# Kernel tuning notes

Hardware: AMD Instinct MI355X
Metric: run time of the kernel (lower is better)

## Reference

```python
import jax, jax.numpy as jnp
import numpy as np

IN_CH = 4096
OUT_CH = 4096
DENSITY = 0.1
BATCH = 8192


def setup_inputs() -> dict:
    key = jax.random.key(0)
    k_mask, k_w, k_b, k_x = jax.random.split(key, 4)
    # Fixed sparsity pattern, as in the torch module's sparse_mask.nonzero()
    mask = jax.random.bernoulli(k_mask, DENSITY, (OUT_CH, IN_CH))
    rows, cols = jnp.nonzero(mask)  # unique (row, col) pairs
    rows = rows.astype(jnp.int32)
    cols = cols.astype(jnp.int32)
    nnz = rows.shape[0]
    # Kaiming-style init per output row (approximate: uniform bound from mean fan-in)
    fan_in = jnp.maximum(jnp.sum(mask, axis=1).astype(jnp.float32), 1.0)  # [OUT_CH]
    gain = np.sqrt(2.0 / (1.0 + 5.0))  # leaky_relu gain with a=sqrt(5)
    std = gain / jnp.sqrt(fan_in)
    w_bound = np.sqrt(3.0) * std  # per-row bound
    u = jax.random.uniform(k_w, (nnz,), minval=-1.0, maxval=1.0)
    sparse_weight = u * w_bound[rows]
    b_bound = 1.0 / jnp.sqrt(fan_in)
    bias = jax.random.uniform(k_b, (OUT_CH,), minval=-1.0, maxval=1.0) * b_bound
    x = jax.random.normal(k_x, (BATCH, IN_CH), dtype=jnp.float32)
    return {
        "x": x,
        "sparse_weight": sparse_weight.astype(jnp.float32),
        "rows": rows,
        "cols": cols,
        "bias": bias.astype(jnp.float32),
    }


def reference(x, sparse_weight, rows, cols, bias):
    # Rebuild the (fixed-pattern) sparse weight as a dense [OUT_CH, IN_CH] matrix
    # (indices are unique, so .set matches the COO semantics), then y = x @ W^T + b.
    W = jnp.zeros((OUT_CH, IN_CH), dtype=sparse_weight.dtype).at[rows, cols].set(sparse_weight)
    return x @ W.T + bias  # [BATCH, OUT_CH]
```

## Files before the change

kernel.cpp:

```cpp
#include <hip/hip_runtime.h>
#include <hip/hip_bf16.h>

#define M_DIM 8192
#define N_DIM 4096
#define K_DIM 4096
#define BM 256
#define BN 128
#define BK 64
#define A_ELEMS (BM * BK)
#define B_ELEMS (BN * BK)
#define LDS_BYTES ((3 * (A_ELEMS + B_ELEMS)) * 2)
#define NT_TILES (K_DIM / BK)

typedef __bf16 bf16x8 __attribute__((ext_vector_type(8)));
typedef float  f32x4  __attribute__((ext_vector_type(4)));
typedef unsigned short u16x8 __attribute__((ext_vector_type(8)));

#define ASYNC16(g, l)                                                          \
  __builtin_amdgcn_global_load_lds(                                            \
      (__attribute__((address_space(1))) void*)(g),                            \
      (__attribute__((address_space(3))) void*)(l), 16, 0, 0)

static __device__ __forceinline__ unsigned short f2bf(float f) {
  unsigned int u = __float_as_uint(f);
  u += 0x7fffu + ((u >> 16) & 1u);
  return (unsigned short)(u >> 16);
}

__global__ __launch_bounds__(256) void sl_prep_bs(
    const float4* __restrict__ x4, u16x8* __restrict__ xb,
    const float* __restrict__ vals, const int* __restrict__ rows,
    const int* __restrict__ cols, unsigned short* __restrict__ W, int nnz) {
  const int b = blockIdx.x;
  if (b < N_DIM) {
    __shared__ __align__(16) unsigned short rowbuf[K_DIM];
    u16x8* rb8 = (u16x8*)rowbuf;
    u16x8 z = {};
    rb8[threadIdx.x] = z;
    rb8[256 + threadIdx.x] = z;
    __syncthreads();
    int l = 0, h = nnz;
    while (l < h) { int m = (l + h) >> 1; if (rows[m] < b) l = m + 1; else h = m; }
    const int s = l;
    h = nnz;
    while (l < h) { int m = (l + h) >> 1; if (rows[m] <= b) l = m + 1; else h = m; }
    const int e = l;
    for (int k = s + threadIdx.x; k < e; k += 256)
      rowbuf[cols[k]] = f2bf(vals[k]);
    __syncthreads();
    u16x8* dst = (u16x8*)(W + (size_t)b * K_DIM);
    dst[threadIdx.x] = rb8[threadIdx.x];
    dst[256 + threadIdx.x] = rb8[256 + threadIdx.x];
  } else {
    const int i = (b - N_DIM) * 256 + threadIdx.x;
    float4 a = x4[2 * i];
    float4 c = x4[2 * i + 1];
    u16x8 o;
    o[0] = f2bf(a.x); o[1] = f2bf(a.y); o[2] = f2bf(a.z); o[3] = f2bf(a.w);
    o[4] = f2bf(c.x); o[5] = f2bf(c.y); o[6] = f2bf(c.z); o[7] = f2bf(c.w);
    xb[i] = o;
  }
}

__global__ __launch_bounds__(512, 2) void sl_gemm_bias(
    const unsigned short* __restrict__ A,
    const unsigned short* __restrict__ B,
    const float* __restrict__ bias,
    float* __restrict__ C) {
  extern __shared__ __align__(16) unsigned short lds[];
  unsigned short* As = lds;
  unsigned short* Bs = lds + 3 * A_ELEMS;

  const int tid  = threadIdx.x;
  const int wave = tid >> 6;
  const int lane = tid & 63;

  const int orig = blockIdx.y * (M_DIM / BM) + blockIdx.x;
  const int swz  = (orig & 7) * 128 + (orig >> 3);
  const int mt   = swz >> 5;
  const int nt   = swz & 31;
  const int m0 = mt * BM;
  const int n0 = nt * BN;

  const int srow = tid >> 3;
  const int scol = ((tid & 7) ^ (srow & 7)) * 8;
  const unsigned short* gA = A + (size_t)(m0 + srow) * K_DIM + scol;
  const unsigned short* gB = B + (size_t)(n0 + srow) * K_DIM + scol;
  const size_t GROW = (size_t)64 * K_DIM;
  const int ldsw = wave * 64 * 8;

  const int wm   = (wave >> 2) * 128;
  const int wn   = (wave & 3) * 32;
  const int fm   = lane & 15;
  const int quad = lane >> 4;
  int offA[8], offB[2], pk[2];
#pragma unroll
  for (int i = 0; i < 8; ++i) offA[i] = (wm + i * 16 + fm) * BK;
#pragma unroll
  for (int i = 0; i < 2; ++i) offB[i] = (wn + i * 16 + fm) * BK;
#pragma unroll
  for (int i = 0; i < 2; ++i) pk[i] = ((i * 4 + quad) ^ (fm & 7)) * 8;

  f32x4 acc[8][2] = {};

#pragma unroll
  for (int tt = 0; tt < 2; ++tt) {
#pragma unroll
    for (int r = 0; r < 4; ++r)
      ASYNC16(gA + tt * BK + r * GROW, As + tt * A_ELEMS + ldsw + r * 4096);
#pragma unroll
    for (int r = 0; r < 2; ++r)
      ASYNC16(gB + tt * BK + r * GROW, Bs + tt * B_ELEMS + ldsw + r * 4096);
  }
  gA += 2 * BK;
  gB += 2 * BK;
  asm volatile("s_waitcnt vmcnt(6)" ::: "memory");
  __builtin_amdgcn_sched_barrier(0);
  __builtin_amdgcn_s_barrier();

#define PHASE(MS, KK, STAGE_CODE, TAIL_CODE)                                   \
  {                                                                            \
    bf16x8 a0 = *(const bf16x8*)(Ac + offA[(MS)*4 + 0] + pk[KK]);              \
    bf16x8 a1 = *(const bf16x8*)(Ac + offA[(MS)*4 + 1] + pk[KK]);              \
    bf16x8 a2 = *(const bf16x8*)(Ac + offA[(MS)*4 + 2] + pk[KK]);              \
    bf16x8 a3 = *(const bf16x8*)(Ac + offA[(MS)*4 + 3] + pk[KK]);              \
    bf16x8 b0 = *(const bf16x8*)(Bc + offB[0] + pk[KK]);                       \
    bf16x8 b1 = *(const bf16x8*)(Bc + offB[1] + pk[KK]);                       \
    STAGE_CODE                                                                 \
    __builtin_amdgcn_s_barrier();                                              \
    asm volatile("s_waitcnt lgkmcnt(0)" ::: "memory");                         \
    __builtin_amdgcn_sched_barrier(0);                                         \
    __builtin_amdgcn_s_setprio(1);                                             \
    acc[(MS)*4+0][0] = __builtin_amdgcn_mfma_f32_16x16x32_bf16(a0, b0, acc[(MS)*4+0][0], 0, 0, 0); \
    acc[(MS)*4+0][1] = __builtin_amdgcn_mfma_f32_16x16x32_bf16(a0, b1, acc[(MS)*4+0][1], 0, 0, 0); \
    acc[(MS)*4+1][0] = __builtin_amdgcn_mfma_f32_16x16x32_bf16(a1, b0, acc[(MS)*4+1][0], 0, 0, 0); \
    acc[(MS)*4+1][1] = __builtin_amdgcn_mfma_f32_16x16x32_bf16(a1, b1, acc[(MS)*4+1][1], 0, 0, 0); \
    acc[(MS)*4+2][0] = __builtin_amdgcn_mfma_f32_16x16x32_bf16(a2, b0, acc[(MS)*4+2][0], 0, 0, 0); \
    acc[(MS)*4+2][1] = __builtin_amdgcn_mfma_f32_16x16x32_bf16(a2, b1, acc[(MS)*4+2][1], 0, 0, 0); \
    acc[(MS)*4+3][0] = __builtin_amdgcn_mfma_f32_16x16x32_bf16(a3, b0, acc[(MS)*4+3][0], 0, 0, 0); \
    acc[(MS)*4+3][1] = __builtin_amdgcn_mfma_f32_16x16x32_bf16(a3, b1, acc[(MS)*4+3][1], 0, 0, 0); \
    __builtin_amdgcn_s_setprio(0);                                             \
    TAIL_CODE                                                                  \
    __builtin_amdgcn_s_barrier();                                              \
  }

  int cur = 0, nxt = 2;
  for (int t = 0; t < NT_TILES; ++t) {
    const unsigned short* Ac = As + cur * A_ELEMS;
    const unsigned short* Bc = Bs + cur * B_ELEMS;
    unsigned short* Asn = As + nxt * A_ELEMS + ldsw;
    unsigned short* Bsn = Bs + nxt * B_ELEMS + ldsw;
    const bool more = (t < NT_TILES - 2);

    PHASE(0, 0,
          if (more) { ASYNC16(gA, Asn); ASYNC16(gA + GROW, Asn + 4096); }, )
    PHASE(0, 1,
          if (more) { ASYNC16(gA + 2 * GROW, Asn + 2 * 4096);
                      ASYNC16(gA + 3 * GROW, Asn + 3 * 4096); }, )
    PHASE(1, 0,
          if (more) { ASYNC16(gB, Bsn); }, )
    PHASE(1, 1,
          if (more) { ASYNC16(gB + GROW, Bsn + 4096); },
          if (more) {
            asm volatile("s_waitcnt vmcnt(6)" ::: "memory");
            __builtin_amdgcn_sched_barrier(0);
          } else if (t == NT_TILES - 2) {
            asm volatile("s_waitcnt vmcnt(0)" ::: "memory");
            __builtin_amdgcn_sched_barrier(0);
          } )

    if (more) { gA += BK; gB += BK; }
    cur = (cur == 2) ? 0 : cur + 1;
    nxt = (nxt == 2) ? 0 : nxt + 1;
  }
#undef PHASE

  float bv[2];
#pragma unroll
  for (int tn = 0; tn < 2; ++tn) bv[tn] = bias[n0 + wn + tn * 16 + fm];

#pragma unroll
  for (int tm = 0; tm < 8; ++tm) {
    const int mbase = m0 + wm + tm * 16 + quad * 4;
#pragma unroll
    for (int tn = 0; tn < 2; ++tn) {
      const int n = n0 + wn + tn * 16 + fm;
      float* p = C + (size_t)mbase * N_DIM + n;
#pragma unroll
      for (int r = 0; r < 4; ++r)
        __builtin_nontemporal_store(acc[tm][tn][r] + bv[tn], p + (size_t)r * N_DIM);
    }
  }
}

__global__ void sl_naive(const float* __restrict__ x, const float* __restrict__ vals,
                         const int* __restrict__ rows, const int* __restrict__ cols,
                         const float* __restrict__ bias, float* __restrict__ out,
                         int nnz) {
  const int o = blockIdx.x;
  int l = 0, h = nnz;
  while (l < h) { int m = (l + h) >> 1; if (rows[m] < o) l = m + 1; else h = m; }
  const int s = l;
  h = nnz;
  while (l < h) { int m = (l + h) >> 1; if (rows[m] <= o) l = m + 1; else h = m; }
  const int e = l;
  const float bv = bias[o];
  for (int b = threadIdx.x; b < M_DIM; b += blockDim.x) {
    float acc = bv;
    const float* xb = x + (size_t)b * K_DIM;
    for (int k = s; k < e; ++k) acc += vals[k] * xb[cols[k]];
    out[(size_t)b * N_DIM + o] = acc;
  }
}

extern "C" void kernel_launch(void* const* d_in, const int* in_sizes, int n_in,
                              void* d_out, int out_size, void* d_ws, size_t ws_size,
                              hipStream_t stream) {
  const float* x    = (const float*)d_in[0];
  const float* vals = (const float*)d_in[1];
  const int*   rows = (const int*)d_in[2];
  const int*   cols = (const int*)d_in[3];
  const float* bias = (const float*)d_in[4];
  float* out = (float*)d_out;
  const int nnz = in_sizes[1];

  const size_t xb_bytes = (size_t)M_DIM * K_DIM * 2;
  const size_t w_bytes  = (size_t)N_DIM * K_DIM * 2;
  const int cvt_blocks  = (M_DIM * K_DIM) / 8 / 256;

  if (ws_size >= xb_bytes + w_bytes) {
    unsigned short* xb = (unsigned short*)d_ws;
    unsigned short* W  = (unsigned short*)((char*)d_ws + xb_bytes);

    static bool attr_done = false;
    if (!attr_done) {
      (void)hipFuncSetAttribute((const void*)sl_gemm_bias,
                                hipFuncAttributeMaxDynamicSharedMemorySize,
                                LDS_BYTES);
      attr_done = true;
    }

    sl_prep_bs<<<N_DIM + cvt_blocks, 256, 0, stream>>>(
        (const float4*)x, (u16x8*)xb, vals, rows, cols, W, nnz);
    sl_gemm_bias<<<dim3(M_DIM / BM, N_DIM / BN), 512, LDS_BYTES, stream>>>(
        xb, W, bias, out);
  } else {
    sl_naive<<<N_DIM, 256, 0, stream>>>(x, vals, rows, cols, bias, out, nnz);
  }
}
```

Before: 549.6 us.

## Enlarge GEMM tile to 256x256 with BK=32 and two-phase pipeline

Widens the block tile from 256x128 to 256x256 and halves BK to 32, so each wave holds an 8x4 grid of MFMA accumulators instead of 8x2. The block swizzle, LDS staging indices and XOR swizzle are reworked for 32-element rows, and the per-tile loop becomes two phases, each prefetching half of the next stage. The goal is to reuse each loaded tile across more MFMAs and cut global and LDS traffic per flop. The cost is doubled accumulator registers, which under launch_bounds(512,2) may cause spills or lower occupancy, plus twice as many barriers per unit of K.

```diff
diff --git a/kernel.cpp b/kernel.cpp
--- a/kernel.cpp
+++ b/kernel.cpp
@@ -5,11 +5,11 @@
 #define N_DIM 4096
 #define K_DIM 4096
 #define BM 256
-#define BN 128
-#define BK 64
+#define BN 256
+#define BK 32
 #define A_ELEMS (BM * BK)
 #define B_ELEMS (BN * BK)
-#define LDS_BYTES ((3 * (A_ELEMS + B_ELEMS)) * 2)
+#define LDS_BYTES (3 * (A_ELEMS + B_ELEMS) * 2)
 #define NT_TILES (K_DIM / BK)
 
 typedef __bf16 bf16x8 __attribute__((ext_vector_type(8)));
@@ -76,73 +76,44 @@
   const int lane = tid & 63;
 
   const int orig = blockIdx.y * (M_DIM / BM) + blockIdx.x;
-  const int swz  = (orig & 7) * 128 + (orig >> 3);
-  const int mt   = swz >> 5;
-  const int nt   = swz & 31;
+  const int swz  = (orig & 7) * 64 + (orig >> 3);
+  const int mt   = swz >> 4;
+  const int nt   = swz & 15;
   const int m0 = mt * BM;
   const int n0 = nt * BN;
 
-  const int srow = tid >> 3;
-  const int scol = ((tid & 7) ^ (srow & 7)) * 8;
+  const int srow = tid >> 2;
+  const int scol = ((tid & 3) ^ (srow & 3)) * 8;
   const unsigned short* gA = A + (size_t)(m0 + srow) * K_DIM + scol;
   const unsigned short* gB = B + (size_t)(n0 + srow) * K_DIM + scol;
-  const size_t GROW = (size_t)64 * K_DIM;
-  const int ldsw = wave * 64 * 8;
+  const size_t GROW = (size_t)128 * K_DIM;
+  const int ldsw = wave * 512;
 
   const int wm   = (wave >> 2) * 128;
-  const int wn   = (wave & 3) * 32;
+  const int wn   = (wave & 3) * 64;
   const int fm   = lane & 15;
   const int quad = lane >> 4;
-  int offA[8], offB[2], pk[2];
-#pragma unroll
-  for (int i = 0; i < 8; ++i) offA[i] = (wm + i * 16 + fm) * BK;
-#pragma unroll
-  for (int i = 0; i < 2; ++i) offB[i] = (wn + i * 16 + fm) * BK;
-#pragma unroll
-  for (int i = 0; i < 2; ++i) pk[i] = ((i * 4 + quad) ^ (fm & 7)) * 8;
-
-  f32x4 acc[8][2] = {};
+  const int pk   = (quad ^ (fm & 3)) * 8;
+  int offA[8], offB[4];
+#pragma unroll
+  for (int i = 0; i < 8; ++i) offA[i] = (wm + i * 16 + fm) * BK + pk;
+#pragma unroll
+  for (int j = 0; j < 4; ++j) offB[j] = (wn + j * 16 + fm) * BK + pk;
+
+  f32x4 acc[8][4] = {};
 
 #pragma unroll
   for (int tt = 0; tt < 2; ++tt) {
-#pragma unroll
-    for (int r = 0; r < 4; ++r)
-      ASYNC16(gA + tt * BK + r * GROW, As + tt * A_ELEMS + ldsw + r * 4096);
-#pragma unroll
-    for (int r = 0; r < 2; ++r)
-      ASYNC16(gB + tt * BK + r * GROW, Bs + tt * B_ELEMS + ldsw + r * 4096);
+    ASYNC16(gA + tt * BK,        As + tt * A_ELEMS + ldsw);
+    ASYNC16(gA + tt * BK + GROW, As + tt * A_ELEMS + 4096 + ldsw);
+    ASYNC16(gB + tt * BK,        Bs + tt * B_ELEMS + ldsw);
+    ASYNC16(gB + tt * BK + GROW, Bs + tt * B_ELEMS + 4096 + ldsw);
   }
   gA += 2 * BK;
   gB += 2 * BK;
-  asm volatile("s_waitcnt vmcnt(6)" ::: "memory");
+  asm volatile("s_waitcnt vmcnt(4)" ::: "memory");
   __builtin_amdgcn_sched_barrier(0);
   __builtin_amdgcn_s_barrier();
-
-#define PHASE(MS, KK, STAGE_CODE, TAIL_CODE)                                   \
-  {                                                                            \
-    bf16x8 a0 = *(const bf16x8*)(Ac + offA[(MS)*4 + 0] + pk[KK]);              \
-    bf16x8 a1 = *(const bf16x8*)(Ac + offA[(MS)*4 + 1] + pk[KK]);              \
-    bf16x8 a2 = *(const bf16x8*)(Ac + offA[(MS)*4 + 2] + pk[KK]);              \
-    bf16x8 a3 = *(const bf16x8*)(Ac + offA[(MS)*4 + 3] + pk[KK]);              \
-    bf16x8 b0 = *(const bf16x8*)(Bc + offB[0] + pk[KK]);                       \
-    bf16x8 b1 = *(const bf16x8*)(Bc + offB[1] + pk[KK]);                       \
-    STAGE_CODE                                                                 \
-    __builtin_amdgcn_s_barrier();                                              \
-    asm volatile("s_waitcnt lgkmcnt(0)" ::: "memory");                         \
-    __builtin_amdgcn_sched_barrier(0);                                         \
-    __builtin_amdgcn_s_setprio(1);                                             \
-    acc[(MS)*4+0][0] = __builtin_amdgcn_mfma_f32_16x16x32_bf16(a0, b0, acc[(MS)*4+0][0], 0, 0, 0); \
-    acc[(MS)*4+0][1] = __builtin_amdgcn_mfma_f32_16x16x32_bf16(a0, b1, acc[(MS)*4+0][1], 0, 0, 0); \
-    acc[(MS)*4+1][0] = __builtin_amdgcn_mfma_f32_16x16x32_bf16(a1, b0, acc[(MS)*4+1][0], 0, 0, 0); \
-    acc[(MS)*4+1][1] = __builtin_amdgcn_mfma_f32_16x16x32_bf16(a1, b1, acc[(MS)*4+1][1], 0, 0, 0); \
-    acc[(MS)*4+2][0] = __builtin_amdgcn_mfma_f32_16x16x32_bf16(a2, b0, acc[(MS)*4+2][0], 0, 0, 0); \
-    acc[(MS)*4+2][1] = __builtin_amdgcn_mfma_f32_16x16x32_bf16(a2, b1, acc[(MS)*4+2][1], 0, 0, 0); \
-    acc[(MS)*4+3][0] = __builtin_amdgcn_mfma_f32_16x16x32_bf16(a3, b0, acc[(MS)*4+3][0], 0, 0, 0); \
-    acc[(MS)*4+3][1] = __builtin_amdgcn_mfma_f32_16x16x32_bf16(a3, b1, acc[(MS)*4+3][1], 0, 0, 0); \
-    __builtin_amdgcn_s_setprio(0);                                             \
-    TAIL_CODE                                                                  \
-    __builtin_amdgcn_s_barrier();                                              \
-  }
 
   int cur = 0, nxt = 2;
   for (int t = 0; t < NT_TILES; ++t) {
@@ -152,38 +123,79 @@
     unsigned short* Bsn = Bs + nxt * B_ELEMS + ldsw;
     const bool more = (t < NT_TILES - 2);
 
-    PHASE(0, 0,
-          if (more) { ASYNC16(gA, Asn); ASYNC16(gA + GROW, Asn + 4096); }, )
-    PHASE(0, 1,
-          if (more) { ASYNC16(gA + 2 * GROW, Asn + 2 * 4096);
-                      ASYNC16(gA + 3 * GROW, Asn + 3 * 4096); }, )
-    PHASE(1, 0,
-          if (more) { ASYNC16(gB, Bsn); }, )
-    PHASE(1, 1,
-          if (more) { ASYNC16(gB + GROW, Bsn + 4096); },
-          if (more) {
-            asm volatile("s_waitcnt vmcnt(6)" ::: "memory");
-            __builtin_amdgcn_sched_barrier(0);
-          } else if (t == NT_TILES - 2) {
-            asm volatile("s_waitcnt vmcnt(0)" ::: "memory");
-            __builtin_amdgcn_sched_barrier(0);
-          } )
+    bf16x8 a0 = *(const bf16x8*)(Ac + offA[0]);
+    bf16x8 a1 = *(const bf16x8*)(Ac + offA[1]);
+    bf16x8 a2 = *(const bf16x8*)(Ac + offA[2]);
+    bf16x8 a3 = *(const bf16x8*)(Ac + offA[3]);
+    bf16x8 b0 = *(const bf16x8*)(Bc + offB[0]);
+    bf16x8 b1 = *(const bf16x8*)(Bc + offB[1]);
+    bf16x8 b2 = *(const bf16x8*)(Bc + offB[2]);
+    bf16x8 b3 = *(const bf16x8*)(Bc + offB[3]);
+    if (more) {
+      ASYNC16(gA, Asn);
+      ASYNC16(gA + GROW, Asn + 4096);
+    }
+    __builtin_amdgcn_sched_barrier(0);
+    __builtin_amdgcn_s_barrier();
+    asm volatile("s_waitcnt lgkmcnt(0)" ::: "memory");
+    __builtin_amdgcn_sched_barrier(0);
+    __builtin_amdgcn_s_setprio(1);
+#pragma unroll
+    for (int j = 0; j < 4; ++j) {
+      bf16x8 bj = (j == 0) ? b0 : (j == 1) ? b1 : (j == 2) ? b2 : b3;
+      acc[0][j] = __builtin_amdgcn_mfma_f32_16x16x32_bf16(a0, bj, acc[0][j], 0, 0, 0);
+      acc[1][j] = __builtin_amdgcn_mfma_f32_16x16x32_bf16(a1, bj, acc[1][j], 0, 0, 0);
+      acc[2][j] = __builtin_amdgcn_mfma_f32_16x16x32_bf16(a2, bj, acc[2][j], 0, 0, 0);
+      acc[3][j] = __builtin_amdgcn_mfma_f32_16x16x32_bf16(a3, bj, acc[3][j], 0, 0, 0);
+    }
+    __builtin_amdgcn_s_setprio(0);
+    __builtin_amdgcn_s_barrier();
+
+    bf16x8 a4 = *(const bf16x8*)(Ac + offA[4]);
+    bf16x8 a5 = *(const bf16x8*)(Ac + offA[5]);
+    bf16x8 a6 = *(const bf16x8*)(Ac + offA[6]);
+    bf16x8 a7 = *(const bf16x8*)(Ac + offA[7]);
+    if (more) {
+      ASYNC16(gB, Bsn);
+      ASYNC16(gB + GROW, Bsn + 4096);
+    }
+    __builtin_amdgcn_sched_barrier(0);
+    __builtin_amdgcn_s_barrier();
+    asm volatile("s_waitcnt lgkmcnt(0)" ::: "memory");
+    __builtin_amdgcn_sched_barrier(0);
+    __builtin_amdgcn_s_setprio(1);
+#pragma unroll
+    for (int j = 0; j < 4; ++j) {
+      bf16x8 bj = (j == 0) ? b0 : (j == 1) ? b1 : (j == 2) ? b2 : b3;
+      acc[4][j] = __builtin_amdgcn_mfma_f32_16x16x32_bf16(a4, bj, acc[4][j], 0, 0, 0);
+      acc[5][j] = __builtin_amdgcn_mfma_f32_16x16x32_bf16(a5, bj, acc[5][j], 0, 0, 0);
+      acc[6][j] = __builtin_amdgcn_mfma_f32_16x16x32_bf16(a6, bj, acc[6][j], 0, 0, 0);
+      acc[7][j] = __builtin_amdgcn_mfma_f32_16x16x32_bf16(a7, bj, acc[7][j], 0, 0, 0);
+    }
+    __builtin_amdgcn_s_setprio(0);
+    if (more) {
+      asm volatile("s_waitcnt vmcnt(4)" ::: "memory");
+      __builtin_amdgcn_sched_barrier(0);
+    } else if (t == NT_TILES - 2) {
+      asm volatile("s_waitcnt vmcnt(0)" ::: "memory");
+      __builtin_amdgcn_sched_barrier(0);
+    }
+    __builtin_amdgcn_s_barrier();
 
     if (more) { gA += BK; gB += BK; }
     cur = (cur == 2) ? 0 : cur + 1;
     nxt = (nxt == 2) ? 0 : nxt + 1;
   }
-#undef PHASE
-
-  float bv[2];
-#pragma unroll
-  for (int tn = 0; tn < 2; ++tn) bv[tn] = bias[n0 + wn + tn * 16 + fm];
+
+  float bv[4];
+#pragma unroll
+  for (int tn = 0; tn < 4; ++tn) bv[tn] = bias[n0 + wn + tn * 16 + fm];
 
 #pragma unroll
   for (int tm = 0; tm < 8; ++tm) {
     const int mbase = m0 + wm + tm * 16 + quad * 4;
 #pragma unroll
-    for (int tn = 0; tn < 2; ++tn) {
+    for (int tn = 0; tn < 4; ++tn) {
       const int n = n0 + wn + tn * 16 + fm;
       float* p = C + (size_t)mbase * N_DIM + n;
 #pragma unroll
```

Measured after the change: 519.3 us. -5.5%, faster.
